# Optimization experiments

Hardware: AMD Instinct MI355X
Metric: run time of the kernel (lower is better)

Reference implementation:

```python
import jax, jax.numpy as jnp
import numpy as np

H = 1152; NH = 16; HD = 72; INTER = 4304; DEPTH = 4
C = 3; T = 2; P = 16; G = 48; M = 2; S = G * G
MERGED = H * M * M; OUT = 2048; ROT = HD // 2  # rotary_pos_emb_dim = head_dim//2


def _ln(x, w, b, eps=1e-6):
    # manual LayerNorm decomposition (mean/var/rsqrt), fp32 like the original
    m = x.mean(-1, keepdims=True)
    xc = x - m
    v = (xc * xc).mean(-1, keepdims=True)
    return w * (xc * jax.lax.rsqrt(v + eps)) + b


def _gelu(x):
    return jax.nn.gelu(x, approximate=True)  # tanh approximation


def _rot_half(x):
    h = x.shape[-1] // 2
    return jnp.concatenate([-x[..., h:], x[..., :h]], axis=-1)


def _pos_ids():
    # Qwen merge-pattern token order: 2x2 spatial blocks are contiguous
    ids = np.arange(G * G).reshape(G // M, M, G // M, M).transpose(0, 2, 1, 3).reshape(-1)
    return jnp.asarray(ids, dtype=jnp.int32)


def setup_inputs() -> dict:
    key = jax.random.key(0)
    ks = jax.random.split(key, 16)
    w = lambda k, shape: jax.random.normal(k, shape, jnp.float32) * 0.02
    return {
        'pixel_values': jax.random.normal(ks[0], (S, C * T * P * P), jnp.float32),
        'cu_seqlens': jnp.array([0, S], jnp.int32),
        'conv_w': w(ks[1], (H, C, T, P, P)),
        'conv_b': jnp.zeros((H,), jnp.float32),
        'pos_tab': w(ks[2], (G * G, H)),
        'ln1_w': jnp.ones((DEPTH, H), jnp.float32), 'ln1_b': jnp.zeros((DEPTH, H), jnp.float32),
        'ln2_w': jnp.ones((DEPTH, H), jnp.float32), 'ln2_b': jnp.zeros((DEPTH, H), jnp.float32),
        'qkv_w': w(ks[3], (DEPTH, 3 * H, H)), 'qkv_b': jnp.zeros((DEPTH, 3 * H), jnp.float32),
        'proj_w': w(ks[4], (DEPTH, H, H)), 'proj_b': jnp.zeros((DEPTH, H), jnp.float32),
        'fc1_w': w(ks[5], (DEPTH, INTER, H)), 'fc1_b': jnp.zeros((DEPTH, INTER), jnp.float32),
        'fc2_w': w(ks[6], (DEPTH, H, INTER)), 'fc2_b': jnp.zeros((DEPTH, H), jnp.float32),
        'm_norm_w': jnp.ones((H,), jnp.float32), 'm_norm_b': jnp.zeros((H,), jnp.float32),
        'm_fc1_w': w(ks[7], (MERGED, MERGED)), 'm_fc1_b': jnp.zeros((MERGED,), jnp.float32),
        'm_fc2_w': w(ks[8], (OUT, MERGED)), 'm_fc2_b': jnp.zeros((OUT,), jnp.float32),
    }


def reference(pixel_values, cu_seqlens, conv_w, conv_b, pos_tab,
              ln1_w, ln1_b, ln2_w, ln2_b, qkv_w, qkv_b, proj_w, proj_b,
              fc1_w, fc1_b, fc2_w, fc2_b, m_norm_w, m_norm_b,
              m_fc1_w, m_fc1_b, m_fc2_w, m_fc2_b):
    pos_ids = _pos_ids()
    # Conv3d with stride == kernel over pre-extracted patches == matmul
    x = pixel_values @ conv_w.reshape(H, -1).T + conv_b            # [S, H]
    x = x + pos_tab[pos_ids]
    # 2D rotary: h-freqs and w-freqs each ROT/2 dims, concat -> ROT, dup -> HD
    inv_freq = 1.0 / (10000.0 ** (jnp.arange(0, ROT, 2, dtype=jnp.float32) / ROT))
    hp = (pos_ids // G).astype(jnp.float32)
    wp = (pos_ids % G).astype(jnp.float32)
    freqs = jnp.concatenate([hp[:, None] * inv_freq, wp[:, None] * inv_freq], axis=-1)  # [S, ROT]
    emb = jnp.concatenate([freqs, freqs], axis=-1)                 # [S, HD]
    cos = jnp.cos(emb)[:, None, :]                                 # [S, 1, HD]
    sin = jnp.sin(emb)[:, None, :]
    # varlen attention: block-diagonal mask from cu_seqlens
    seg = jnp.searchsorted(cu_seqlens, jnp.arange(S), side='right')
    mask = jnp.where(seg[:, None] == seg[None, :], 0.0, -1e9).astype(jnp.float32)
    scale = 1.0 / np.sqrt(HD)
    for i in range(DEPTH):
        h = _ln(x, ln1_w[i], ln1_b[i])
        qkv = (h @ qkv_w[i].T + qkv_b[i]).reshape(S, 3, NH, HD)
        q, k, v = qkv[:, 0], qkv[:, 1], qkv[:, 2]
        q = q * cos + _rot_half(q) * sin
        k = k * cos + _rot_half(k) * sin
        scores = jnp.einsum('qhd,khd->hqk', q, k) * scale + mask
        attn = jax.nn.softmax(scores, axis=-1)
        o = jnp.einsum('hqk,khd->qhd', attn, v).reshape(S, H)
        x = x + o @ proj_w[i].T + proj_b[i]
        h2 = _ln(x, ln2_w[i], ln2_b[i])
        x = x + _gelu(h2 @ fc1_w[i].T + fc1_b[i]) @ fc2_w[i].T + fc2_b[i]
    # patch merger: pre-merge LN -> reshape to merged -> fc1 -> gelu(tanh) -> fc2
    y = _ln(x, m_norm_w, m_norm_b).reshape(-1, MERGED)             # [S/4, MERGED]
    return _gelu(y @ m_fc1_w.T + m_fc1_b) @ m_fc2_w.T + m_fc2_b   # [S/4, OUT]
```

## Files before the change

### kernel.cpp

```cpp
#include <hip/hip_runtime.h>
#include <hip/hip_bf16.h>
#include <math.h>

#define S 2304
#define HDIM 1152
#define NHEAD 16
#define HD 72
#define INTER 4304
#define INTERP 4352
#define DEPTH 4
#define MERGED 4608
#define OUTD 2048
#define KIN 1536
#define NSPLIT 4
#define KHALF (S / NSPLIT)

typedef float f4 __attribute__((ext_vector_type(4)));
typedef short s8v __attribute__((ext_vector_type(8)));

__device__ __forceinline__ int pos_id_of(int s) {
  int a = s / 96;
  int r = s % 96;
  int b = r >> 2;
  int c = (r >> 1) & 1;
  int d = r & 1;
  return a * 96 + c * 48 + b * 2 + d;
}

__device__ __forceinline__ float gelu_f(float v) {
  const float c = 0.7978845608028654f;
  float t = tanhf(c * (v + 0.044715f * v * v * v));
  return 0.5f * v * (1.f + t);
}

__device__ __forceinline__ unsigned short f2b(float f) {
  unsigned int u = __float_as_uint(f);
  u += 0x7fffu + ((u >> 16) & 1u);
  return (unsigned short)(u >> 16);
}
__device__ __forceinline__ float b2f(unsigned short u) {
  return __uint_as_float(((unsigned int)u) << 16);
}

__device__ __forceinline__ void gload16(const void* g, void* l) {
  __builtin_amdgcn_global_load_lds(
      (const __attribute__((address_space(1))) void*)g,
      (__attribute__((address_space(3))) void*)l, 16, 0, 0);
}

__device__ __forceinline__ int xcd_swz(int flat, int nwg) {
  int q = nwg >> 3, r8 = nwg & 7;
  int xcd = flat & 7, lin = flat >> 3;
  return (xcd < r8 ? xcd * (q + 1) : r8 * (q + 1) + (xcd - r8) * q) + lin;
}

__global__ void __launch_bounds__(256) cvt_kernel(
    const float* __restrict__ src, unsigned short* __restrict__ dst,
    int N, int Ksrc, int Kdst)
{
  int idx = blockIdx.x * 256 + threadIdx.x;
  int kc = Kdst >> 3;
  if (idx >= N * kc) return;
  int r = idx / kc;
  int c8 = (idx % kc) << 3;
  const float* sp = src + (size_t)r * Ksrc + c8;
  unsigned short outv[8];
#pragma unroll
  for (int e = 0; e < 8; ++e)
    outv[e] = (c8 + e < Ksrc) ? f2b(sp[e]) : (unsigned short)0;
  *(uint4*)(dst + (size_t)r * Kdst + c8) = *(uint4*)outv;
}

__global__ void __launch_bounds__(256) gemm_bf16_m64_kernel(
    const unsigned short* __restrict__ A, const unsigned short* __restrict__ B,
    const float* __restrict__ bias, void* __restrict__ Cout,
    int M, int Nreal, int K, int lda, int ldb, int ldc, int act, int outbf)
{
  __shared__ unsigned short Asm[2][64 * 32];
  __shared__ unsigned short Bsm[2][128 * 32];
  const int tid = threadIdx.x;
  const int lane = tid & 63;
  const int wv = tid >> 6;

  int flat = blockIdx.y * gridDim.x + blockIdx.x;
  int swz = xcd_swz(flat, gridDim.x * gridDim.y);
  const int bm = (swz / gridDim.x) * 64;
  const int bn = (swz % gridDim.x) * 128;

  const int g8 = (lane >> 4) << 3;
  const int lr = lane & 15;

  const int lrow = lane >> 2;
  const int kq = (lane & 3) << 3;
  const unsigned short* AgP = A + (size_t)(bm + wv * 16 + lrow) * lda + kq;
  int brow1 = bn + wv * 16 + lrow;      if (brow1 >= Nreal) brow1 = Nreal - 1;
  int brow2 = bn + 64 + wv * 16 + lrow; if (brow2 >= Nreal) brow2 = Nreal - 1;
  const unsigned short* BgP1 = B + (size_t)brow1 * ldb + kq;
  const unsigned short* BgP2 = B + (size_t)brow2 * ldb + kq;

  f4 acc[4][2];
#pragma unroll
  for (int m = 0; m < 4; ++m)
#pragma unroll
    for (int n = 0; n < 2; ++n) { acc[m][n].x = 0.f; acc[m][n].y = 0.f; acc[m][n].z = 0.f; acc[m][n].w = 0.f; }

  const int nt = K >> 5;
  gload16(AgP, &Asm[0][(wv * 16) * 32]);
  gload16(BgP1, &Bsm[0][(wv * 16) * 32]);
  gload16(BgP2, &Bsm[0][(64 + wv * 16) * 32]);
  asm volatile("s_waitcnt vmcnt(0)" ::: "memory");
  __syncthreads();

  int cur = 0;
  for (int t = 0; t < nt; ++t) {
    if (t + 1 < nt) {
      int ko = (t + 1) << 5;
      gload16(AgP + ko, &Asm[cur ^ 1][(wv * 16) * 32]);
      gload16(BgP1 + ko, &Bsm[cur ^ 1][(wv * 16) * 32]);
      gload16(BgP2 + ko, &Bsm[cur ^ 1][(64 + wv * 16) * 32]);
    }
    s8v af[4], bf[2];
#pragma unroll
    for (int m = 0; m < 4; ++m)
      af[m] = *(const s8v*)&Asm[cur][(m * 16 + lr) * 32 + g8];
#pragma unroll
    for (int n = 0; n < 2; ++n)
      bf[n] = *(const s8v*)&Bsm[cur][(wv * 32 + n * 16 + lr) * 32 + g8];
#pragma unroll
    for (int m = 0; m < 4; ++m)
#pragma unroll
      for (int n = 0; n < 2; ++n)
        acc[m][n] = __builtin_amdgcn_mfma_f32_16x16x32_bf16(af[m], bf[n], acc[m][n], 0, 0, 0);
    asm volatile("s_waitcnt vmcnt(0)" ::: "memory");
    __syncthreads();
    cur ^= 1;
  }

  const int g4 = (lane >> 4) << 2;
#pragma unroll
  for (int m = 0; m < 4; ++m) {
    int r = bm + m * 16 + g4;
#pragma unroll
    for (int n = 0; n < 2; ++n) {
      int cidx = bn + wv * 32 + n * 16 + lr;
      float bb = (cidx < Nreal) ? bias[cidx] : 0.f;
#pragma unroll
      for (int j = 0; j < 4; ++j) {
        int rr = r + j;
        float v = acc[m][n][j] + bb;
        if (act) v = gelu_f(v);
        if (cidx >= Nreal) v = 0.f;
        if (outbf) ((unsigned short*)Cout)[(size_t)rr * ldc + cidx] = f2b(v);
        else       ((float*)Cout)[(size_t)rr * ldc + cidx] = v;
      }
    }
  }
}

__global__ void __launch_bounds__(256) gemm_bf16_splitk_kernel(
    const unsigned short* __restrict__ A, const unsigned short* __restrict__ B,
    float* __restrict__ Cpart, int M, int N, int Kc, int lda, int ldb)
{
  __shared__ unsigned short Asm[2][128 * 32];
  __shared__ unsigned short Bsm[2][128 * 32];
  const int tid = threadIdx.x;
  const int lane = tid & 63;
  const int wv = tid >> 6;
  const int wr = wv >> 1, wc = wv & 1;

  int flat = blockIdx.y * gridDim.x + blockIdx.x;
  int swz = xcd_swz(flat, gridDim.x * gridDim.y);
  const int bm = (swz / gridDim.x) * 128;
  const int bn = (swz % gridDim.x) * 128;
  const int z = blockIdx.z;
  const int kbase = z * Kc;

  const int g8 = (lane >> 4) << 3;
  const int lr = lane & 15;

  const int srow = wv * 32 + (lane >> 2);
  const int kcol = (lane & 3) << 3;
  int ar0 = bm + srow;      if (ar0 >= M) ar0 = M - 1;
  int ar1 = bm + srow + 16; if (ar1 >= M) ar1 = M - 1;
  int br0 = bn + srow;      if (br0 >= N) br0 = N - 1;
  int br1 = bn + srow + 16; if (br1 >= N) br1 = N - 1;
  const unsigned short* Ag0 = A + (size_t)ar0 * lda + kbase + kcol;
  const unsigned short* Ag1 = A + (size_t)ar1 * lda + kbase + kcol;
  const unsigned short* Bg0 = B + (size_t)br0 * ldb + kbase + kcol;
  const unsigned short* Bg1 = B + (size_t)br1 * ldb + kbase + kcol;

  f4 acc[4][4];
#pragma unroll
  for (int m = 0; m < 4; ++m)
#pragma unroll
    for (int n = 0; n < 4; ++n) { acc[m][n].x = 0.f; acc[m][n].y = 0.f; acc[m][n].z = 0.f; acc[m][n].w = 0.f; }

  const int nt = Kc >> 5;
  gload16(Ag0, &Asm[0][(wv * 32) * 32]);
  gload16(Ag1, &Asm[0][(wv * 32 + 16) * 32]);
  gload16(Bg0, &Bsm[0][(wv * 32) * 32]);
  gload16(Bg1, &Bsm[0][(wv * 32 + 16) * 32]);
  asm volatile("s_waitcnt vmcnt(0)" ::: "memory");
  __syncthreads();

  int cur = 0;
  for (int t = 0; t < nt; ++t) {
    if (t + 1 < nt) {
      int ko = (t + 1) << 5;
      gload16(Ag0 + ko, &Asm[cur ^ 1][(wv * 32) * 32]);
      gload16(Ag1 + ko, &Asm[cur ^ 1][(wv * 32 + 16) * 32]);
      gload16(Bg0 + ko, &Bsm[cur ^ 1][(wv * 32) * 32]);
      gload16(Bg1 + ko, &Bsm[cur ^ 1][(wv * 32 + 16) * 32]);
    }
    s8v af[4], bf[4];
#pragma unroll
    for (int m = 0; m < 4; ++m)
      af[m] = *(const s8v*)&Asm[cur][(wr * 64 + m * 16 + lr) * 32 + g8];
#pragma unroll
    for (int n = 0; n < 4; ++n)
      bf[n] = *(const s8v*)&Bsm[cur][(wc * 64 + n * 16 + lr) * 32 + g8];
#pragma unroll
    for (int m = 0; m < 4; ++m)
#pragma unroll
      for (int n = 0; n < 4; ++n)
        acc[m][n] = __builtin_amdgcn_mfma_f32_16x16x32_bf16(af[m], bf[n], acc[m][n], 0, 0, 0);
    asm volatile("s_waitcnt vmcnt(0)" ::: "memory");
    __syncthreads();
    cur ^= 1;
  }

  float* Cz = Cpart + (size_t)z * M * N;
  const int g4 = (lane >> 4) << 2;
#pragma unroll
  for (int m = 0; m < 4; ++m) {
    int r = bm + wr * 64 + m * 16 + g4;
#pragma unroll
    for (int n = 0; n < 4; ++n) {
      int cidx = bn + wc * 64 + n * 16 + lr;
      if (cidx < N) {
#pragma unroll
        for (int j = 0; j < 4; ++j) {
          int rr = r + j;
          if (rr < M) Cz[(size_t)rr * N + cidx] = acc[m][n][j];
        }
      }
    }
  }
}

__global__ void __launch_bounds__(256) combine_gemm_kernel(
    const float* __restrict__ Cpart, int nz, const float* __restrict__ bias,
    const float* __restrict__ resid, float* __restrict__ out, int M, int N)
{
  int idx = blockIdx.x * 256 + threadIdx.x;
  int total = (M * N) >> 2;
  if (idx >= total) return;
  int r = idx / (N >> 2);
  int c4 = (idx % (N >> 2)) << 2;
  size_t off = (size_t)r * N + c4;
  float4 s = *(const float4*)(Cpart + off);
  for (int z = 1; z < nz; ++z) {
    float4 p = *(const float4*)(Cpart + (size_t)z * M * N + off);
    s.x += p.x; s.y += p.y; s.z += p.z; s.w += p.w;
  }
  float4 b = *(const float4*)(bias + c4);
  s.x += b.x; s.y += b.y; s.z += b.z; s.w += b.w;
  if (resid) {
    float4 rv = *(const float4*)(resid + off);
    s.x += rv.x; s.y += rv.y; s.z += rv.z; s.w += rv.w;
  }
  *(float4*)(out + off) = s;
}

__global__ void __launch_bounds__(256) combine_ln_kernel(
    const float* __restrict__ Cpart, int nz, const float* __restrict__ bias,
    const float* __restrict__ resid, const float* __restrict__ pos_tab,
    float* __restrict__ xout, const float* __restrict__ lnw,
    const float* __restrict__ lnb, unsigned short* __restrict__ hout)
{
  __shared__ float red[8];
  const int row = blockIdx.x;
  const int tid = threadIdx.x;
  const float* pos = pos_tab ? pos_tab + (size_t)pos_id_of(row) * HDIM : nullptr;
  float v[5];
  float s1 = 0.f;
#pragma unroll
  for (int t = 0; t < 5; ++t) {
    int i = tid + t * 256;
    float s = 0.f;
    if (i < HDIM) {
      size_t off = (size_t)row * HDIM + i;
      s = Cpart[off];
      for (int z = 1; z < nz; ++z) s += Cpart[(size_t)z * ((size_t)S * HDIM) + off];
      s += bias[i];
      if (resid) s += resid[off];
      if (pos) s += pos[i];
      xout[off] = s;
    }
    v[t] = s;
    s1 += s;
  }
#pragma unroll
  for (int off = 32; off > 0; off >>= 1) s1 += __shfl_down(s1, off);
  if ((tid & 63) == 0) red[tid >> 6] = s1;
  __syncthreads();
  float mean = (red[0] + red[1] + red[2] + red[3]) * (1.f / HDIM);
  float s2 = 0.f;
#pragma unroll
  for (int t = 0; t < 5; ++t) {
    int i = tid + t * 256;
    if (i < HDIM) { float d = v[t] - mean; s2 += d * d; }
  }
#pragma unroll
  for (int off = 32; off > 0; off >>= 1) s2 += __shfl_down(s2, off);
  __syncthreads();
  if ((tid & 63) == 0) red[tid >> 6] = s2;
  __syncthreads();
  float var = (red[0] + red[1] + red[2] + red[3]) * (1.f / HDIM);
  float rstd = rsqrtf(var + 1e-6f);
#pragma unroll
  for (int t = 0; t < 5; ++t) {
    int i = tid + t * 256;
    if (i < HDIM)
      hout[(size_t)row * HDIM + i] = f2b(lnw[i] * ((v[t] - mean) * rstd) + lnb[i]);
  }
}

__global__ void rope_tables_kernel(float* __restrict__ cosT, float* __restrict__ sinT)
{
  int s = blockIdx.x;
  int j = threadIdx.x;
  if (j >= 36) return;
  int pid = pos_id_of(s);
  float hp = (float)(pid / 48);
  float wp = (float)(pid % 48);
  int f = (j < 18) ? j : (j - 18);
  float inv = powf(10000.f, -(2.f * (float)f) / 36.f);
  float ang = ((j < 18) ? hp : wp) * inv;
  cosT[s * 36 + j] = cosf(ang);
  sinT[s * 36 + j] = sinf(ang);
}

__global__ void seg_kernel(const int* __restrict__ cu, int n_cu, int* __restrict__ seg)
{
  int i = blockIdx.x * 256 + threadIdx.x;
  if (i >= S) return;
  int s = 0;
  for (int t = 0; t < n_cu; ++t) s += (cu[t] <= i) ? 1 : 0;
  seg[i] = s;
}

__global__ void __launch_bounds__(256) rope_kernel(unsigned short* __restrict__ qkv,
    const float* __restrict__ cosT, const float* __restrict__ sinT)
{
  int idx = blockIdx.x * 256 + threadIdx.x;
  int d = idx % 36; int t = idx / 36;
  int hh = t % NHEAD; t /= NHEAD;
  int qk = t & 1; int s = t >> 1;
  unsigned short* base = qkv + (size_t)s * 3456 + qk * 1152 + hh * 72;
  float c = cosT[s * 36 + d], sn = sinT[s * 36 + d];
  float x0 = b2f(base[d]), x1 = b2f(base[d + 36]);
  base[d] = f2b(x0 * c - x1 * sn);
  base[d + 36] = f2b(x1 * c + x0 * sn);
}

#define KT 64
#define KSL 88
#define ASCALE 0.11785113019775793f

__global__ void __launch_bounds__(256) flash_mfma_kernel(
    const unsigned short* __restrict__ qkv, unsigned short* __restrict__ opart,
    float* __restrict__ ml, const int* __restrict__ seg)
{
  __shared__ __align__(16) unsigned short Ks[64 * KSL];
  __shared__ __align__(16) unsigned short Vt[80 * 72];
  __shared__ __align__(16) unsigned short Ps[4][16 * 72];

  const int tid = threadIdx.x;
  const int lane = tid & 63;
  const int wv = tid >> 6;
  const int g = lane >> 4;
  const int c = lane & 15;

  int flat = (blockIdx.z * NHEAD + blockIdx.y) * (S / 128) + blockIdx.x;
  int swz = xcd_swz(flat, (S / 128) * NHEAD * NSPLIT);
  const int q0 = (swz % (S / 128)) * 128;
  const int hh = (swz / (S / 128)) % NHEAD;
  const int sidx = swz / ((S / 128) * NHEAD);
  const int kbeg = sidx * KHALF;
  const int qr = q0 + wv * 32;

  for (int i = tid; i < 64 * 8; i += 256) {
    int r = i >> 3, cc = i & 7;
    *(unsigned int*)&Ks[r * KSL + 72 + cc * 2] = 0u;
  }
  for (int i = tid; i < 288; i += 256)
    *(unsigned int*)&Vt[72 * 72 + i * 2] = 0u;

  const bool uni = (seg[q0] == seg[q0 + 127]) && (seg[kbeg] == seg[kbeg + KHALF - 1])
                && (seg[q0] == seg[kbeg]);
  const int msgA = seg[qr + c];
  const int msgB = seg[qr + 16 + c];

  s8v qfA[3], qfB[3];
  {
    const unsigned short* qa = qkv + (size_t)(qr + c) * 3456 + hh * HD;
    const unsigned short* qb = qkv + (size_t)(qr + 16 + c) * 3456 + hh * HD;
#pragma unroll
    for (int ks = 0; ks < 3; ++ks) {
      int k = ks * 32 + g * 8;
      if (k <= 64) { qfA[ks] = *(const s8v*)(qa + k); qfB[ks] = *(const s8v*)(qb + k); }
      else {
        s8v z;
#pragma unroll
        for (int t = 0; t < 8; ++t) z[t] = 0;
        qfA[ks] = z; qfB[ks] = z;
      }
    }
  }

  float mA = -1e30f, lA = 0.f, mB = -1e30f, lB = 0.f;
  f4 accoA[5], accoB[5];
#pragma unroll
  for (int n = 0; n < 5; ++n) {
    accoA[n].x = 0.f; accoA[n].y = 0.f; accoA[n].z = 0.f; accoA[n].w = 0.f;
    accoB[n].x = 0.f; accoB[n].y = 0.f; accoB[n].z = 0.f; accoB[n].w = 0.f;
  }

  uint4 kreg[3], vreg[3];

#define STAGE_LOAD(KT0)                                                                  \
  {                                                                                      \
    _Pragma("unroll")                                                                    \
    for (int ii = 0; ii < 3; ++ii) {                                                     \
      int idx = tid + ii * 256;                                                          \
      if (idx < 576) {                                                                   \
        int rK = idx / 9, cK = idx % 9;                                                  \
        kreg[ii] = *(const uint4*)(qkv + (size_t)((KT0) + rK) * 3456 + 1152 + hh * HD + cK * 8); \
        int rV = idx & 63, cV = idx >> 6;                                                \
        vreg[ii] = *(const uint4*)(qkv + (size_t)((KT0) + rV) * 3456 + 2304 + hh * HD + cV * 8); \
      }                                                                                  \
    }                                                                                    \
  }

#define STAGE_WRITE()                                                                    \
  {                                                                                      \
    _Pragma("unroll")                                                                    \
    for (int ii = 0; ii < 3; ++ii) {                                                     \
      int idx = tid + ii * 256;                                                          \
      if (idx < 576) {                                                                   \
        int rK = idx / 9, cK = idx % 9;                                                  \
        *(uint4*)&Ks[rK * KSL + cK * 8] = kreg[ii];                                      \
        int rV = idx & 63, cV = idx >> 6;                                                \
        unsigned short vv[8];                                                            \
        *(uint4*)vv = vreg[ii];                                                          \
        _Pragma("unroll")                                                                \
        for (int e = 0; e < 8; ++e) Vt[(cV * 8 + e) * 72 + rV] = vv[e];                  \
      }                                                                                  \
    }                                                                                    \
  }

#define SUBBLOCK(QF, MSG, MM, LL, ACCO, ROWOFF)                                          \
  {                                                                                      \
    f4 accs[4];                                                                          \
    _Pragma("unroll")                                                                    \
    for (int nk = 0; nk < 4; ++nk) { accs[nk].x = 0.f; accs[nk].y = 0.f; accs[nk].z = 0.f; accs[nk].w = 0.f; } \
    _Pragma("unroll")                                                                    \
    for (int ks = 0; ks < 3; ++ks) {                                                     \
      const int koff = (ks < 2) ? (ks * 32 + g * 8) : 64;                                \
      _Pragma("unroll")                                                                  \
      for (int nk = 0; nk < 4; ++nk) {                                                   \
        s8v bk = *(const s8v*)&Ks[(nk * 16 + c) * KSL + koff];                           \
        accs[nk] = __builtin_amdgcn_mfma_f32_16x16x32_bf16(bk, QF[ks], accs[nk], 0, 0, 0); \
      }                                                                                  \
    }                                                                                    \
    float sc[4][4];                                                                      \
    float mx = -1e30f;                                                                   \
    if (uni) {                                                                           \
      _Pragma("unroll")                                                                  \
      for (int nk = 0; nk < 4; ++nk)                                                     \
        _Pragma("unroll")                                                                \
        for (int j = 0; j < 4; ++j) {                                                    \
          float vv = accs[nk][j] * ASCALE;                                               \
          sc[nk][j] = vv; mx = fmaxf(mx, vv);                                            \
        }                                                                                \
    } else {                                                                             \
      _Pragma("unroll")                                                                  \
      for (int nk = 0; nk < 4; ++nk)                                                     \
        _Pragma("unroll")                                                                \
        for (int j = 0; j < 4; ++j) {                                                    \
          int kk = k0 + nk * 16 + g * 4 + j;                                             \
          float vv = accs[nk][j] * ASCALE + ((seg[kk] == MSG) ? 0.f : -1e9f);             \
          sc[nk][j] = vv; mx = fmaxf(mx, vv);                                            \
        }                                                                                \
    }                                                                                    \
    mx = fmaxf(mx, __shfl_xor(mx, 16));                                                  \
    mx = fmaxf(mx, __shfl_xor(mx, 32));                                                  \
    float mn = fmaxf(MM, mx);                                                            \
    float al = __expf(MM - mn);                                                          \
    MM = mn;                                                                             \
    float rsum = 0.f;                                                                    \
    float p[4][4];                                                                       \
    _Pragma("unroll")                                                                    \
    for (int nk = 0; nk < 4; ++nk)                                                       \
      _Pragma("unroll")                                                                  \
      for (int j = 0; j < 4; ++j) {                                                      \
        float pv = __expf(sc[nk][j] - mn);                                               \
        p[nk][j] = pv; rsum += pv;                                                       \
      }                                                                                  \
    rsum += __shfl_xor(rsum, 16);                                                        \
    rsum += __shfl_xor(rsum, 32);                                                        \
    LL = LL * al + rsum;                                                                 \
    _Pragma("unroll")                                                                    \
    for (int nk = 0; nk < 4; ++nk) {                                                     \
      unsigned int w0 = (unsigned int)f2b(p[nk][0]) | ((unsigned int)f2b(p[nk][1]) << 16); \
      unsigned int w1 = (unsigned int)f2b(p[nk][2]) | ((unsigned int)f2b(p[nk][3]) << 16); \
      uint2 wv2; wv2.x = w0; wv2.y = w1;                                                 \
      *(uint2*)&Ps[wv][c * 72 + nk * 16 + g * 4] = wv2;                                  \
    }                                                                                    \
    float alpha_row[4];                                                                  \
    _Pragma("unroll")                                                                    \
    for (int j = 0; j < 4; ++j)                                                          \
      alpha_row[j] = __shfl(al, (lane & 48) | (g * 4 + j));                              \
    _Pragma("unroll")                                                                    \
    for (int n = 0; n < 5; ++n)                                                          \
      _Pragma("unroll")                                                                  \
      for (int j = 0; j < 4; ++j) ACCO[n][j] *= alpha_row[j];                            \
    asm volatile("s_waitcnt lgkmcnt(0)" ::: "memory");                                   \
    __builtin_amdgcn_sched_barrier(0);                                                   \
    _Pragma("unroll")                                                                    \
    for (int ks = 0; ks < 2; ++ks) {                                                     \
      s8v pa = *(const s8v*)&Ps[wv][c * 72 + ks * 32 + g * 8];                           \
      _Pragma("unroll")                                                                  \
      for (int n = 0; n < 5; ++n) {                                                      \
        s8v vb = *(const s8v*)&Vt[(n * 16 + c) * 72 + ks * 32 + g * 8];                  \
        ACCO[n] = __builtin_amdgcn_mfma_f32_16x16x32_bf16(pa, vb, ACCO[n], 0, 0, 0);     \
      }                                                                                  \
    }                                                                                    \
  }

  STAGE_LOAD(kbeg);
  asm volatile("s_waitcnt vmcnt(0)" ::: "memory");
  STAGE_WRITE();
  asm volatile("s_waitcnt lgkmcnt(0)" ::: "memory");
  __builtin_amdgcn_s_barrier();
  __builtin_amdgcn_sched_barrier(0);

  for (int k0 = kbeg; k0 < kbeg + KHALF; k0 += KT) {
    const bool more = (k0 + KT < kbeg + KHALF);
    if (more) STAGE_LOAD(k0 + KT);

    SUBBLOCK(qfA, msgA, mA, lA, accoA, 0);
    SUBBLOCK(qfB, msgB, mB, lB, accoB, 16);

    asm volatile("s_waitcnt lgkmcnt(0)" ::: "memory");
    __builtin_amdgcn_s_barrier();
    if (more) {
      asm volatile("s_waitcnt vmcnt(0)" ::: "memory");
      STAGE_WRITE();
      asm volatile("s_waitcnt lgkmcnt(0)" ::: "memory");
    }
    __builtin_amdgcn_s_barrier();
    __builtin_amdgcn_sched_barrier(0);
  }

  unsigned short* op = opart + (size_t)(sidx * NHEAD + hh) * S * 72;
  float lrA[4], mrA[4], lrB[4], mrB[4];
#pragma unroll
  for (int j = 0; j < 4; ++j) {
    int src = (lane & 48) | (g * 4 + j);
    lrA[j] = __shfl(lA, src); mrA[j] = __shfl(mA, src);
    lrB[j] = __shfl(lB, src); mrB[j] = __shfl(mB, src);
  }
#pragma unroll
  for (int n = 0; n < 5; ++n) {
    int col = n * 16 + c;
    if (col < HD) {
#pragma unroll
      for (int j = 0; j < 4; ++j) {
        int rowA = qr + g * 4 + j;
        op[(size_t)rowA * 72 + col] = f2b(accoA[n][j]);
        op[(size_t)(rowA + 16) * 72 + col] = f2b(accoB[n][j]);
      }
    }
  }
  if (c == 0) {
#pragma unroll
    for (int j = 0; j < 4; ++j) {
      int rowA = qr + g * 4 + j;
      float2 va; va.x = mrA[j]; va.y = lrA[j];
      *(float2*)&ml[((size_t)(sidx * NHEAD + hh) * S + rowA) * 2] = va;
      float2 vb; vb.x = mrB[j]; vb.y = lrB[j];
      *(float2*)&ml[((size_t)(sidx * NHEAD + hh) * S + rowA + 16) * 2] = vb;
    }
  }
}

__global__ void __launch_bounds__(256) attn_combine_kernel(
    const unsigned short* __restrict__ opart, const float* __restrict__ ml,
    unsigned short* __restrict__ oout)
{
  int idx = blockIdx.x * 256 + threadIdx.x;
  int d = idx % 72;
  int row = (idx / 72) % S;
  int hh = idx / (72 * S);
  float mv[NSPLIT], lv[NSPLIT];
  float ms = -1e30f;
#pragma unroll
  for (int z = 0; z < NSPLIT; ++z) {
    size_t b = (size_t)(z * NHEAD + hh) * S + row;
    mv[z] = ml[b * 2]; lv[z] = ml[b * 2 + 1];
    ms = fmaxf(ms, mv[z]);
  }
  float l = 0.f, o = 0.f;
#pragma unroll
  for (int z = 0; z < NSPLIT; ++z) {
    size_t b = (size_t)(z * NHEAD + hh) * S + row;
    float a = __expf(mv[z] - ms);
    l += a * lv[z];
    o += a * b2f(opart[b * 72 + d]);
  }
  oout[(size_t)row * HDIM + hh * 72 + d] = f2b(o / l);
}

extern "C" void kernel_launch(void* const* d_in, const int* in_sizes, int n_in,
                              void* d_out, int out_size, void* d_ws, size_t ws_size,
                              hipStream_t stream)
{
  (void)n_in; (void)out_size; (void)ws_size;
  const float* pix    = (const float*)d_in[0];
  const int*   cu     = (const int*)d_in[1];
  const int    n_cu   = in_sizes[1];
  const float* conv_w = (const float*)d_in[2];
  const float* conv_b = (const float*)d_in[3];
  const float* pos_tab= (const float*)d_in[4];
  const float* ln1_w  = (const float*)d_in[5];
  const float* ln1_b  = (const float*)d_in[6];
  const float* ln2_w  = (const float*)d_in[7];
  const float* ln2_b  = (const float*)d_in[8];
  const float* qkv_w  = (const float*)d_in[9];
  const float* qkv_b  = (const float*)d_in[10];
  const float* proj_w = (const float*)d_in[11];
  const float* proj_b = (const float*)d_in[12];
  const float* fc1_w  = (const float*)d_in[13];
  const float* fc1_b  = (const float*)d_in[14];
  const float* fc2_w  = (const float*)d_in[15];
  const float* fc2_b  = (const float*)d_in[16];
  const float* mn_w   = (const float*)d_in[17];
  const float* mn_b   = (const float*)d_in[18];
  const float* mf1_w  = (const float*)d_in[19];
  const float* mf1_b  = (const float*)d_in[20];
  const float* mf2_w  = (const float*)d_in[21];
  const float* mf2_b  = (const float*)d_in[22];
  float* out = (float*)d_out;

  float*    x      = (float*)d_ws;
  unsigned short* h_bf   = (unsigned short*)(x + (size_t)S * HDIM);
  unsigned short* qkv_bf = h_bf + (size_t)S * HDIM;
  unsigned short* A_bf   = qkv_bf + (size_t)S * 3456;
  unsigned short* Wbuf   = A_bf + (size_t)S * INTERP;
  float*    cosT   = (float*)(Wbuf + (size_t)MERGED * MERGED);
  float*    sinT   = cosT + (size_t)S * 36;
  int*      seg    = (int*)(sinT + (size_t)S * 36);
  unsigned short* pix_bf = A_bf;
  unsigned short* opart  = A_bf;
  float*    ml     = (float*)(A_bf + (size_t)NSPLIT * NHEAD * S * 72);
  float*    part_h = (float*)h_bf;
  float*    part_q = (float*)qkv_bf;

  auto cvt = [&](const float* src, unsigned short* dst, int N, int Ksrc, int Kdst) {
    int total = N * (Kdst >> 3);
    cvt_kernel<<<(total + 255) / 256, 256, 0, stream>>>(src, dst, N, Ksrc, Kdst);
  };
  auto gemm64 = [&](const unsigned short* A, const unsigned short* B, const float* bias,
                    void* C, int M, int N, int K, int lda, int ldb, int ldc, int act, int outbf) {
    gemm_bf16_m64_kernel<<<dim3((N + 127) / 128, M / 64), 256, 0, stream>>>(
        A, B, bias, C, M, N, K, lda, ldb, ldc, act, outbf);
  };
  auto splitk = [&](const unsigned short* A, const unsigned short* B, float* part,
                    int M, int N, int K, int nz, int lda, int ldb) {
    gemm_bf16_splitk_kernel<<<dim3(N / 128, (M + 127) / 128, nz), 256, 0, stream>>>(
        A, B, part, M, N, K / nz, lda, ldb);
  };
  auto comb_ln = [&](float* part, int nz, const float* bias, const float* resid,
                     const float* pos, const float* lw, const float* lb) {
    combine_ln_kernel<<<S, 256, 0, stream>>>(part, nz, bias, resid, pos, x, lw, lb, h_bf);
  };

  cvt(pix, pix_bf, S, KIN, KIN);
  cvt(conv_w, Wbuf, HDIM, KIN, KIN);
  splitk(pix_bf, Wbuf, part_h, S, HDIM, KIN, 2, KIN, KIN);
  rope_tables_kernel<<<S, 64, 0, stream>>>(cosT, sinT);
  seg_kernel<<<(S + 255) / 256, 256, 0, stream>>>(cu, n_cu, seg);
  comb_ln(part_h, 2, conv_b, nullptr, pos_tab, ln1_w, ln1_b);

  for (int layer = 0; layer < DEPTH; ++layer) {
    cvt(qkv_w + (size_t)layer * 3456 * HDIM, Wbuf, 3456, HDIM, HDIM);
    gemm64(h_bf, Wbuf, qkv_b + layer * 3456, qkv_bf, S, 3456, HDIM, HDIM, HDIM, 3456, 0, 1);
    rope_kernel<<<(S * 2 * NHEAD * 36) / 256, 256, 0, stream>>>(qkv_bf, cosT, sinT);
    flash_mfma_kernel<<<dim3(S / 128, NHEAD, NSPLIT), 256, 0, stream>>>(qkv_bf, opart, ml, seg);
    attn_combine_kernel<<<(NHEAD * S * 72) / 256, 256, 0, stream>>>(opart, ml, h_bf);
    cvt(proj_w + (size_t)layer * HDIM * HDIM, Wbuf, HDIM, HDIM, HDIM);
    splitk(h_bf, Wbuf, part_q, S, HDIM, HDIM, 3, HDIM, HDIM);
    comb_ln(part_q, 3, proj_b + layer * HDIM, x, nullptr,
            ln2_w + layer * HDIM, ln2_b + layer * HDIM);
    cvt(fc1_w + (size_t)layer * INTER * HDIM, Wbuf, INTER, HDIM, HDIM);
    gemm64(h_bf, Wbuf, fc1_b + layer * INTER, A_bf, S, INTER, HDIM, HDIM, HDIM, INTERP, 1, 1);
    cvt(fc2_w + (size_t)layer * HDIM * INTER, Wbuf, HDIM, INTER, INTERP);
    splitk(A_bf, Wbuf, part_h, S, HDIM, INTERP, 2, INTERP, INTERP);
    if (layer < DEPTH - 1)
      comb_ln(part_h, 2, fc2_b + layer * HDIM, x, nullptr,
              ln1_w + (layer + 1) * HDIM, ln1_b + (layer + 1) * HDIM);
    else
      comb_ln(part_h, 2, fc2_b + layer * HDIM, x, nullptr, mn_w, mn_b);
  }

  cvt(mf1_w, Wbuf, MERGED, MERGED, MERGED);
  gemm64(h_bf, Wbuf, mf1_b, A_bf, 576, MERGED, MERGED, MERGED, MERGED, MERGED, 1, 1);
  cvt(mf2_w, Wbuf, OUTD, MERGED, MERGED);
  splitk(A_bf, Wbuf, part_h, 576, OUTD, MERGED, 4, MERGED, MERGED);
  combine_gemm_kernel<<<((576 * OUTD / 4) + 255) / 256, 256, 0, stream>>>(
      part_h, 4, mf2_b, nullptr, out, 576, OUTD);
}
```

Baseline: 1.741 ms.

## XOR-swizzle attention LDS tiles and skip softmax rescale when max is stable

The flash attention kernel replaces the padded K/V/P shared-memory layouts with XOR-swizzled 80-wide rows so MFMA fragment reads avoid bank conflicts. It also adds a lazy-rescale rule: when every row's new block max stays within 8 of the running max across the wavefront, the running max, alpha and accumulator rescaling are skipped. The swizzle adds index arithmetic on the stage writes. The lazy rescale lets exponentials grow up to e^8 before renormalisation, which is safe in fp32 but relies on that bound.

Measured after the change: 1.734 ms. About the same (-0.4%).

```diff
diff --git a/kernel.cpp b/kernel.cpp
--- a/kernel.cpp
+++ b/kernel.cpp
@@ -365,22 +365,22 @@
 }
 
 #define KT 64
-#define KSL 88
 #define ASCALE 0.11785113019775793f
 
 __global__ void __launch_bounds__(256) flash_mfma_kernel(
     const unsigned short* __restrict__ qkv, unsigned short* __restrict__ opart,
     float* __restrict__ ml, const int* __restrict__ seg)
 {
-  __shared__ __align__(16) unsigned short Ks[64 * KSL];
-  __shared__ __align__(16) unsigned short Vt[80 * 72];
-  __shared__ __align__(16) unsigned short Ps[4][16 * 72];
+  __shared__ __align__(16) unsigned short Ks[64 * 80];
+  __shared__ __align__(16) unsigned short Vt[80 * 80];
+  __shared__ __align__(16) unsigned short Ps[4][16 * 80];
 
   const int tid = threadIdx.x;
   const int lane = tid & 63;
   const int wv = tid >> 6;
   const int g = lane >> 4;
   const int c = lane & 15;
+  const int cm = c & 7;
 
   int flat = (blockIdx.z * NHEAD + blockIdx.y) * (S / 128) + blockIdx.x;
   int swz = xcd_swz(flat, (S / 128) * NHEAD * NSPLIT);
@@ -390,12 +390,8 @@
   const int kbeg = sidx * KHALF;
   const int qr = q0 + wv * 32;
 
-  for (int i = tid; i < 64 * 8; i += 256) {
-    int r = i >> 3, cc = i & 7;
-    *(unsigned int*)&Ks[r * KSL + 72 + cc * 2] = 0u;
-  }
-  for (int i = tid; i < 288; i += 256)
-    *(unsigned int*)&Vt[72 * 72 + i * 2] = 0u;
+  for (int i = tid; i < 320; i += 256)
+    ((unsigned int*)&Vt[72 * 80])[i] = 0u;
 
   const bool uni = (seg[q0] == seg[q0 + 127]) && (seg[kbeg] == seg[kbeg + KHALF - 1])
                 && (seg[q0] == seg[kbeg]);
@@ -450,27 +446,31 @@
       int idx = tid + ii * 256;                                                          \
       if (idx < 576) {                                                                   \
         int rK = idx / 9, cK = idx % 9;                                                  \
-        *(uint4*)&Ks[rK * KSL + cK * 8] = kreg[ii];                                      \
+        int colx = (cK < 8) ? ((cK ^ (rK & 7)) << 3) : 64;                               \
+        *(uint4*)&Ks[rK * 80 + colx] = kreg[ii];                                         \
         int rV = idx & 63, cV = idx >> 6;                                                \
         unsigned short vv[8];                                                            \
         *(uint4*)vv = vreg[ii];                                                          \
         _Pragma("unroll")                                                                \
-        for (int e = 0; e < 8; ++e) Vt[(cV * 8 + e) * 72 + rV] = vv[e];                  \
+        for (int e = 0; e < 8; ++e) {                                                    \
+          int drow = cV * 8 + e;                                                         \
+          Vt[drow * 80 + (rV ^ ((drow & 7) << 3))] = vv[e];                              \
+        }                                                                                \
       }                                                                                  \
     }                                                                                    \
   }
 
-#define SUBBLOCK(QF, MSG, MM, LL, ACCO, ROWOFF)                                          \
+#define SUBBLOCK(QF, MSG, MM, LL, ACCO)                                                  \
   {                                                                                      \
     f4 accs[4];                                                                          \
     _Pragma("unroll")                                                                    \
     for (int nk = 0; nk < 4; ++nk) { accs[nk].x = 0.f; accs[nk].y = 0.f; accs[nk].z = 0.f; accs[nk].w = 0.f; } \
     _Pragma("unroll")                                                                    \
     for (int ks = 0; ks < 3; ++ks) {                                                     \
-      const int koff = (ks < 2) ? (ks * 32 + g * 8) : 64;                                \
+      const int koff = (ks < 2) ? (((ks * 4 + g) ^ cm) << 3) : 64;                       \
       _Pragma("unroll")                                                                  \
       for (int nk = 0; nk < 4; ++nk) {                                                   \
-        s8v bk = *(const s8v*)&Ks[(nk * 16 + c) * KSL + koff];                           \
+        s8v bk = *(const s8v*)&Ks[(nk * 16 + c) * 80 + koff];                            \
         accs[nk] = __builtin_amdgcn_mfma_f32_16x16x32_bf16(bk, QF[ks], accs[nk], 0, 0, 0); \
       }                                                                                  \
     }                                                                                    \
@@ -496,16 +496,20 @@
     }                                                                                    \
     mx = fmaxf(mx, __shfl_xor(mx, 16));                                                  \
     mx = fmaxf(mx, __shfl_xor(mx, 32));                                                  \
-    float mn = fmaxf(MM, mx);                                                            \
-    float al = __expf(MM - mn);                                                          \
-    MM = mn;                                                                             \
+    const bool allkeep = __all(mx <= MM + 8.0f);                                         \
+    float al = 1.0f;                                                                     \
+    if (!allkeep) {                                                                      \
+      float mn = fmaxf(MM, mx);                                                          \
+      al = __expf(MM - mn);                                                              \
+      MM = mn;                                                                           \
+    }                                                                                    \
     float rsum = 0.f;                                                                    \
     float p[4][4];                                                                       \
     _Pragma("unroll")                                                                    \
     for (int nk = 0; nk < 4; ++nk)                                                       \
       _Pragma("unroll")                                                                  \
       for (int j = 0; j < 4; ++j) {                                                      \
-        float pv = __expf(sc[nk][j] - mn);                                               \
+        float pv = __expf(sc[nk][j] - MM);                                               \
         p[nk][j] = pv; rsum += pv;                                                       \
       }                                                                                  \
     rsum += __shfl_xor(rsum, 16);                                                        \
@@ -516,24 +520,27 @@
       unsigned int w0 = (unsigned int)f2b(p[nk][0]) | ((unsigned int)f2b(p[nk][1]) << 16); \
       unsigned int w1 = (unsigned int)f2b(p[nk][2]) | ((unsigned int)f2b(p[nk][3]) << 16); \
       uint2 wv2; wv2.x = w0; wv2.y = w1;                                                 \
-      *(uint2*)&Ps[wv][c * 72 + nk * 16 + g * 4] = wv2;                                  \
+      *(uint2*)&Ps[wv][c * 80 + ((nk * 16 + g * 4) ^ (cm << 3))] = wv2;                  \
     }                                                                                    \
-    float alpha_row[4];                                                                  \
-    _Pragma("unroll")                                                                    \
-    for (int j = 0; j < 4; ++j)                                                          \
-      alpha_row[j] = __shfl(al, (lane & 48) | (g * 4 + j));                              \
-    _Pragma("unroll")                                                                    \
-    for (int n = 0; n < 5; ++n)                                                          \
+    if (!allkeep) {                                                                      \
+      float alpha_row[4];                                                                \
       _Pragma("unroll")                                                                  \
-      for (int j = 0; j < 4; ++j) ACCO[n][j] *= alpha_row[j];                            \
+      for (int j = 0; j < 4; ++j)                                                        \
+        alpha_row[j] = __shfl(al, (lane & 48) | (g * 4 + j));                            \
+      _Pragma("unroll")                                                                  \
+      for (int n = 0; n < 5; ++n)                                                        \
+        _Pragma("unroll")                                                                \
+        for (int j = 0; j < 4; ++j) ACCO[n][j] *= alpha_row[j];                          \
+    }                                                                                    \
     asm volatile("s_waitcnt lgkmcnt(0)" ::: "memory");                                   \
     __builtin_amdgcn_sched_barrier(0);                                                   \
     _Pragma("unroll")                                                                    \
     for (int ks = 0; ks < 2; ++ks) {                                                     \
-      s8v pa = *(const s8v*)&Ps[wv][c * 72 + ks * 32 + g * 8];                           \
+      const int poff = ((ks * 4 + g) ^ cm) << 3;                                         \
+      s8v pa = *(const s8v*)&Ps[wv][c * 80 + poff];                                      \
       _Pragma("unroll")                                                                  \
       for (int n = 0; n < 5; ++n) {                                                      \
-        s8v vb = *(const s8v*)&Vt[(n * 16 + c) * 72 + ks * 32 + g * 8];                  \
+        s8v vb = *(const s8v*)&Vt[(n * 16 + c) * 80 + poff];                             \
         ACCO[n] = __builtin_amdgcn_mfma_f32_16x16x32_bf16(pa, vb, ACCO[n], 0, 0, 0);     \
       }                                                                                  \
     }                                                                                    \
@@ -550,8 +557,8 @@
     const bool more = (k0 + KT < kbeg + KHALF);
     if (more) STAGE_LOAD(k0 + KT);
 
-    SUBBLOCK(qfA, msgA, mA, lA, accoA, 0);
-    SUBBLOCK(qfB, msgB, mB, lB, accoB, 16);
+    SUBBLOCK(qfA, msgA, mA, lA, accoA);
+    SUBBLOCK(qfB, msgB, mB, lB, accoB);
 
     asm volatile("s_waitcnt lgkmcnt(0)" ::: "memory");
     __builtin_amdgcn_s_barrier();
```
